# Optimization experiments

Hardware: AMD Instinct MI355X
Metric: run time of the kernel (lower is better)

Reference implementation:

```python
import jax, jax.numpy as jnp
import numpy as np

NA = 3          # anchors per head
NC = 3          # classes (labels < 3 are valid)
IGNORE_THRES = 0.5
OBJ_SCALE = 5.0
NOOBJ_SCALE = 0.5
GRIDS = [19, 38, 76]
SCALED_ANCHORS = [
    jnp.array([[116., 90.], [156., 198.], [373., 326.]], jnp.float32) / 32.0,  # large head
    jnp.array([[30., 61.], [62., 45.], [59., 119.]], jnp.float32) / 16.0,      # medium head
    jnp.array([[10., 13.], [16., 30.], [33., 23.]], jnp.float32) / 8.0,        # small head
]


def _safe_log(p):
    # torch BCELoss clamps log terms at -100
    return jnp.maximum(jnp.log(p), -100.0)


def _bce(p, t):
    return -(t * _safe_log(p) + (1.0 - t) * _safe_log(1.0 - p))


def _scale_loss(yolo_out, boxes, labels, anchors, G):
    B = yolo_out.shape[0]
    out = yolo_out.reshape(B, NA, G, G, -1)            # [B,3,G,G,8]
    aw = anchors[:, 0].reshape(1, NA, 1, 1)
    ah = anchors[:, 1].reshape(1, NA, 1, 1)
    # _change_bbox
    px = out[..., 0] - jnp.floor(out[..., 0])
    py = out[..., 1] - jnp.floor(out[..., 1])
    pw = jnp.log(out[..., 2] / aw + 1e-16)
    ph = jnp.log(out[..., 3] / ah + 1e-16)
    pconf = out[..., 4]
    pcls = out[..., 5:]                                 # [B,3,G,G,NC]
    # _yolo_targets (vectorized; boxes occupy distinct grid cells by construction)
    tb = boxes * G                                      # [B,nb,4]
    valid = labels < NC                                 # [B,nb]
    vf = valid.astype(out.dtype)
    gi = jnp.clip(tb[..., 0].astype(jnp.int32), 0, G - 1)
    gj = jnp.clip(tb[..., 1].astype(jnp.int32), 0, G - 1)
    bw, bh = tb[..., 2], tb[..., 3]                     # [B,nb]
    # anchor-wh IoU (same formula incl. 1e-16 placement as source)
    inter = jnp.minimum(anchors[:, 0], bw[..., None]) * jnp.minimum(anchors[:, 1], bh[..., None])
    union = anchors[:, 0] * anchors[:, 1] + 1e-16 + (bw * bh)[..., None] - inter
    iou = inter / union                                 # [B,nb,NA]
    best = jnp.argmax(iou, axis=-1)                     # [B,nb]
    bidx = jnp.arange(B)[:, None]                       # [B,1] -> broadcasts with [B,nb]
    obj = jnp.zeros((B, NA, G, G), out.dtype).at[bidx, best, gj, gi].max(vf)
    is_best = best[..., None] == jnp.arange(NA)         # [B,nb,NA]
    clear = valid[..., None] & ((iou > IGNORE_THRES) | is_best)
    keep = 1.0 - clear.astype(out.dtype)
    noobj = jnp.ones((B, NA, G, G), out.dtype).at[
        bidx[..., None], jnp.arange(NA), gj[..., None], gi[..., None]].min(keep)
    # tx/ty in the source are t_x - t_x.float() == 0, so targets stay zero
    twv = vf * jnp.log(bw / anchors[best, 0] + 1e-16)
    thv = vf * jnp.log(bh / anchors[best, 1] + 1e-16)
    tw = jnp.zeros((B, NA, G, G), out.dtype).at[bidx, best, gj, gi].set(twv)
    th = jnp.zeros((B, NA, G, G), out.dtype).at[bidx, best, gj, gi].set(thv)
    tcls = jnp.zeros((B, NA, G, G, NC), out.dtype).at[
        bidx, best, gj, gi, jnp.clip(labels, 0, NC - 1)].max(vf)
    tconf = obj
    # masked sum losses (reduction='sum' over masked elements)
    x_loss = jnp.sum(obj * px ** 2)
    y_loss = jnp.sum(obj * py ** 2)
    w_loss = jnp.sum(obj * (pw - tw) ** 2)
    h_loss = jnp.sum(obj * (ph - th) ** 2)
    conf_obj = jnp.sum(obj * _bce(pconf, tconf))
    conf_noobj = jnp.sum(noobj * _bce(pconf, tconf))
    cls_loss = jnp.sum(obj[..., None] * _bce(pcls, tcls))
    return (x_loss + y_loss + w_loss + h_loss
            + OBJ_SCALE * conf_obj + NOOBJ_SCALE * conf_noobj + cls_loss)


def reference(out_large, out_medium, out_small, boxes, labels):
    B = out_large.shape[0]
    loss = 0.0
    for out, anc, g in zip((out_large, out_medium, out_small), SCALED_ANCHORS, GRIDS):
        loss = loss + _scale_loss(out, boxes, labels, anc, g)
    return loss / B


def setup_inputs() -> dict:
    key = jax.random.key(0)
    ks = jax.random.split(key, 8)
    B, NB = 128, 12
    # predictions in (0.02, 0.98): valid BCE probs and positive w/h
    def u(k, shape):
        return 0.02 + 0.96 * jax.random.uniform(k, shape, jnp.float32)
    out_large = u(ks[0], (B, 3 * 19 * 19, 8))
    out_medium = u(ks[1], (B, 3 * 38 * 38, 8))
    out_small = u(ks[2], (B, 3 * 76 * 76, 8))
    # box centers: distinct grid columns per box at all grid sizes
    base_x = (jnp.arange(NB, dtype=jnp.float32) + 0.5) / NB
    xc = base_x[None, :] + jax.random.uniform(ks[3], (B, NB), jnp.float32, -0.004, 0.004)
    yc = jax.random.uniform(ks[4], (B, NB), jnp.float32, 0.1, 0.9)
    wh = jax.random.uniform(ks[5], (B, NB, 2), jnp.float32, 0.05, 0.4)
    boxes = jnp.concatenate([xc[..., None], yc[..., None], wh], axis=-1)
    labels = jax.random.randint(ks[6], (B, NB), 0, 5, jnp.int32)  # labels>=3 invalid
    return {"out_large": out_large, "out_medium": out_medium, "out_small": out_small,
            "boxes": boxes, "labels": labels}
```

## Files before the change

### kernel.cpp

```cpp
#include <hip/hip_runtime.h>

#define NA 3
#define NCLS 3
#define NB 12
#define BATCH 128
#define UNITS 1792

__device__ __constant__ float AWc[3][3] = {{3.625f, 4.875f, 11.65625f},
                                           {1.875f, 3.875f, 3.6875f},
                                           {1.25f,  2.0f,   4.125f}};
__device__ __constant__ float AHc[3][3] = {{2.8125f, 6.1875f, 10.1875f},
                                           {3.8125f, 2.8125f, 7.4375f},
                                           {1.625f,  3.75f,   2.875f}};

__device__ __forceinline__ float safelog(float x) {
    return fmaxf(__logf(x), -100.0f);
}


template <int G, int S>
__device__ __forceinline__ float cell_loss(int c, float4 q0, float4 q1,
                                           const int* rk, const float* sdat) {
    constexpr int GG = G * G;
    int a   = c / GG;
    int rem = c - a * GG;

    float keepv = 1.0f;
    int objn = -1;
#pragma unroll
    for (int n = 0; n < NB; n++) {
        int pk = rk[n];
        bool hit = ((pk & 0xFFFF) == rem);
        int fl = pk >> 16;
        if (hit && ((fl >> a) & 1)) keepv = 0.0f;
        if (hit && ((fl >> (4 + a)) & 1)) objn = n;
    }

    float conf = q1.x;
    float loss = -0.5f * keepv * safelog(1.0f - conf);

    if (objn >= 0) {
        int pk = rk[objn];
        int cls = (pk >> 24) & 3;
        float tw = sdat[objn], th = sdat[NB + objn];
        float aws = AWc[S][a], ahs = AHc[S][a];
        float px = q0.x - floorf(q0.x);
        float py = q0.y - floorf(q0.y);
        float pw = __logf(q0.z / aws + 1e-16f);
        float ph = __logf(q0.w / ahs + 1e-16f);
        float dw = pw - tw, dh = ph - th;
        loss += px * px + py * py + dw * dw + dh * dh;
        loss += -5.0f * safelog(conf);
        float c0 = q1.y, c1 = q1.z, c2 = q1.w;
        loss -= (cls == 0) ? safelog(c0) : safelog(1.0f - c0);
        loss -= (cls == 1) ? safelog(c1) : safelog(1.0f - c1);
        loss -= (cls == 2) ? safelog(c2) : safelog(1.0f - c2);
    }
    return loss;
}

template <int G, int S, int ITER>
__device__ __forceinline__ float scale_body(int b, int chunk,
        const float* __restrict__ outp,
        const float* __restrict__ boxes,
        const int* __restrict__ labels,
        int* skey, float* sdat)
{
    constexpr int GG = G * G;
    constexpr int CELLS = NA * GG;
    const int tid = threadIdx.x;

    if (tid < NB) {
        float4 bx = ((const float4*)boxes)[b * NB + tid];
        int lab = labels[b * NB + tid];
        bool valid = lab < NCLS;

        float bw = bx.z * (float)G, bh = bx.w * (float)G;
        int gi = min(max((int)(bx.x * (float)G), 0), G - 1);
        int gj = min(max((int)(bx.y * (float)G), 0), G - 1);

        float iou[3]; int best = 0; float bi = -1.0f;
#pragma unroll
        for (int a = 0; a < 3; a++) {
            float aw = AWc[S][a], ah = AHc[S][a];
            float inter = fminf(aw, bw) * fminf(ah, bh);
            float uni = aw * ah + 1e-16f + bw * bh - inter;
            iou[a] = inter / uni;
            if (iou[a] > bi) { bi = iou[a]; best = a; }
        }
        int flags = 0;
        if (valid) {
#pragma unroll
            for (int a = 0; a < 3; a++)
                if (iou[a] > 0.5f || a == best) flags |= (1 << a);
            flags |= (1 << (4 + best));
        }
        int cls = min(max(lab, 0), NCLS - 1);
        skey[tid] = (gj * G + gi) | (flags << 16) | (cls << 24);
        sdat[tid]      = valid ? __logf(bw / AWc[S][best] + 1e-16f) : 0.0f;
        sdat[NB + tid] = valid ? __logf(bh / AHc[S][best] + 1e-16f) : 0.0f;
    }
    __syncthreads();

    int rk[NB];
#pragma unroll
    for (int n = 0; n < NB; n++) rk[n] = __builtin_amdgcn_readfirstlane(skey[n]);

    const float* outb = outp + (size_t)b * CELLS * 8;
    float acc = 0.0f;
    const int base = chunk * (256 * ITER);

#pragma unroll
    for (int kb = 0; kb < ITER; kb += 4) {
        float4 Q0[4], Q1[4];
        int cs[4];
#pragma unroll
        for (int j = 0; j < 4; j++) {
            if (kb + j < ITER) {
                int c = base + (kb + j) * 256 + tid;
                cs[j] = c;
                int cc = (c < CELLS) ? c : (CELLS - 1);
                const float* cp = outb + (size_t)cc * 8;
                Q0[j] = *(const float4*)cp;
                Q1[j] = *(const float4*)(cp + 4);
            }
        }
#pragma unroll
        for (int j = 0; j < 4; j++) {
            if (kb + j < ITER) {
                float L = cell_loss<G, S>((cs[j] < CELLS) ? cs[j] : (CELLS - 1),
                                          Q0[j], Q1[j], rk, sdat);
                acc += (cs[j] < CELLS) ? L : 0.0f;
            }
        }
    }
    return acc;
}

__launch_bounds__(256)
__global__ void fused_loss(const float* __restrict__ oL,
                           const float* __restrict__ oM,
                           const float* __restrict__ oS,
                           const float* __restrict__ boxes,
                           const int* __restrict__ labels,
                           float* __restrict__ partials)
{
    __shared__ int skey[NB];
    __shared__ float sdat[2 * NB];
    __shared__ float red[256];

    const int u = blockIdx.x;
    const int tid = threadIdx.x;

    float acc;
    if (u < 128) {
        acc = scale_body<19, 0, 5>(u, 0, oL, boxes, labels, skey, sdat);
    } else if (u < 640) {
        int r = u - 128;
        acc = scale_body<38, 1, 5>(r >> 2, r & 3, oM, boxes, labels, skey, sdat);
    } else {
        int r = u - 640;
        acc = scale_body<76, 2, 8>(r / 9, r % 9, oS, boxes, labels, skey, sdat);
    }

    red[tid] = acc;
    __syncthreads();
#pragma unroll
    for (int s = 128; s > 0; s >>= 1) {
        if (tid < s) red[tid] += red[tid + s];
        __syncthreads();
    }
    if (tid == 0) partials[u] = red[0];
}

__global__ void final_reduce(const float* __restrict__ partials,
                             float* __restrict__ out) {
    __shared__ float red[256];
    const int tid = threadIdx.x;
    float acc = 0.0f;
#pragma unroll
    for (int i = 0; i < 7; i++) acc += partials[tid + i * 256];
    red[tid] = acc;
    __syncthreads();
#pragma unroll
    for (int s = 128; s > 0; s >>= 1) {
        if (tid < s) red[tid] += red[tid + s];
        __syncthreads();
    }
    if (tid == 0) out[0] = red[0] * (1.0f / (float)BATCH);
}

extern "C" void kernel_launch(void* const* d_in, const int* in_sizes, int n_in,
                              void* d_out, int out_size, void* d_ws, size_t ws_size,
                              hipStream_t stream) {
    const float* oL     = (const float*)d_in[0];
    const float* oM     = (const float*)d_in[1];
    const float* oS     = (const float*)d_in[2];
    const float* boxes  = (const float*)d_in[3];
    const int*   labels = (const int*)d_in[4];

    float* partials = (float*)d_ws;

    fused_loss<<<UNITS, 256, 0, stream>>>(oL, oM, oS, boxes, labels, partials);
    final_reduce<<<1, 256, 0, stream>>>(partials, (float*)d_out);
}
```

Measured before the change: 25.55 us.

## Split loss into dense no-object stream plus sparse per-box corrections

Measured after the change: 24.76 us. 3.1% less time.

```diff
diff --git a/kernel.cpp b/kernel.cpp
--- a/kernel.cpp
+++ b/kernel.cpp
@@ -4,7 +4,16 @@
 #define NCLS 3
 #define NB 12
 #define BATCH 128
-#define UNITS 1792
+
+#define NL_CELLS (128 * 1083)
+#define NM_CELLS (128 * 4332)
+#define NS_CELLS (128 * 17328)
+#define NTOT (NL_CELLS + NM_CELLS + NS_CELLS)
+
+#define CORR_BLOCKS 384
+#define STREAM_BLOCKS 1536
+#define UNITS (CORR_BLOCKS + STREAM_BLOCKS)
+#define STRIDE (STREAM_BLOCKS * 256)
 
 __device__ __constant__ float AWc[3][3] = {{3.625f, 4.875f, 11.65625f},
                                            {1.875f, 3.875f, 3.6875f},
@@ -17,124 +26,75 @@
     return fmaxf(__logf(x), -100.0f);
 }
 
+template <int G, int S>
+__device__ __forceinline__ float corr_body(int b, const float* __restrict__ outp,
+                                           const float* __restrict__ boxes,
+                                           const int* __restrict__ labels) {
+    constexpr int GG = G * G;
+    constexpr int CELLS = NA * GG;
+    const int l = threadIdx.x;
+    const int n = l / 3, a = l - n * 3;
+    const bool active = (l < 36);
+    const int nn = active ? n : 0;
 
-template <int G, int S>
-__device__ __forceinline__ float cell_loss(int c, float4 q0, float4 q1,
-                                           const int* rk, const float* sdat) {
-    constexpr int GG = G * G;
-    int a   = c / GG;
-    int rem = c - a * GG;
+    float4 bx = ((const float4*)boxes)[b * NB + nn];
+    int lab = labels[b * NB + nn];
+    bool valid = active && (lab < NCLS);
 
-    float keepv = 1.0f;
-    int objn = -1;
+    float bw = bx.z * (float)G, bh = bx.w * (float)G;
+    int gi = min(max((int)(bx.x * (float)G), 0), G - 1);
+    int gj = min(max((int)(bx.y * (float)G), 0), G - 1);
+
+    float iou[3]; int best = 0; float bi = -1.0f;
 #pragma unroll
-    for (int n = 0; n < NB; n++) {
-        int pk = rk[n];
-        bool hit = ((pk & 0xFFFF) == rem);
-        int fl = pk >> 16;
-        if (hit && ((fl >> a) & 1)) keepv = 0.0f;
-        if (hit && ((fl >> (4 + a)) & 1)) objn = n;
+    for (int aa = 0; aa < 3; aa++) {
+        float aw = AWc[S][aa], ah = AHc[S][aa];
+        float inter = fminf(aw, bw) * fminf(ah, bh);
+        float uni = aw * ah + 1e-16f + bw * bh - inter;
+        iou[aa] = inter / uni;
+        if (iou[aa] > bi) { bi = iou[aa]; best = aa; }
+    }
+    bool cleared = valid && (iou[a] > 0.5f || a == best);
+    bool isobj   = valid && (a == best);
+
+    unsigned key = (unsigned)(a * GG + gj * G + gi);
+    unsigned v = key | (cleared ? 0x100000u : 0u) | (isobj ? 0x200000u : 0u);
+
+    bool dupc = false, notwin = false;
+#pragma unroll
+    for (int j = 0; j < 36; j++) {
+        unsigned vj = (unsigned)__shfl((int)v, j);
+        bool same = ((vj ^ v) & 0xFFFFFu) == 0u;
+        dupc   = dupc   || (same && (vj & 0x100000u) && j < l);
+        notwin = notwin || (same && (vj & 0x200000u) && j > l);
     }
 
-    float conf = q1.x;
-    float loss = -0.5f * keepv * safelog(1.0f - conf);
+    float corr = 0.0f;
+    const float* cellp = outp + ((size_t)b * CELLS + key) * 8;
 
-    if (objn >= 0) {
-        int pk = rk[objn];
-        int cls = (pk >> 24) & 3;
-        float tw = sdat[objn], th = sdat[NB + objn];
-        float aws = AWc[S][a], ahs = AHc[S][a];
+    if (cleared && !dupc) {
+        float conf = cellp[4];
+        corr += 0.5f * safelog(1.0f - conf);
+    }
+    if (isobj && !notwin) {
+        float4 q0 = *(const float4*)cellp;
+        float4 q1 = *(const float4*)(cellp + 4);
+        float aw = AWc[S][a], ah = AHc[S][a];
+        float tw = __logf(bw / aw + 1e-16f);
+        float th = __logf(bh / ah + 1e-16f);
         float px = q0.x - floorf(q0.x);
         float py = q0.y - floorf(q0.y);
-        float pw = __logf(q0.z / aws + 1e-16f);
-        float ph = __logf(q0.w / ahs + 1e-16f);
+        float pw = __logf(q0.z / aw + 1e-16f);
+        float ph = __logf(q0.w / ah + 1e-16f);
         float dw = pw - tw, dh = ph - th;
-        loss += px * px + py * py + dw * dw + dh * dh;
-        loss += -5.0f * safelog(conf);
-        float c0 = q1.y, c1 = q1.z, c2 = q1.w;
-        loss -= (cls == 0) ? safelog(c0) : safelog(1.0f - c0);
-        loss -= (cls == 1) ? safelog(c1) : safelog(1.0f - c1);
-        loss -= (cls == 2) ? safelog(c2) : safelog(1.0f - c2);
+        float conf = q1.x;
+        corr += px * px + py * py + dw * dw + dh * dh;
+        corr -= 5.0f * safelog(conf);
+        corr -= (lab == 0) ? safelog(q1.y) : safelog(1.0f - q1.y);
+        corr -= (lab == 1) ? safelog(q1.z) : safelog(1.0f - q1.z);
+        corr -= (lab == 2) ? safelog(q1.w) : safelog(1.0f - q1.w);
     }
-    return loss;
-}
-
-template <int G, int S, int ITER>
-__device__ __forceinline__ float scale_body(int b, int chunk,
-        const float* __restrict__ outp,
-        const float* __restrict__ boxes,
-        const int* __restrict__ labels,
-        int* skey, float* sdat)
-{
-    constexpr int GG = G * G;
-    constexpr int CELLS = NA * GG;
-    const int tid = threadIdx.x;
-
-    if (tid < NB) {
-        float4 bx = ((const float4*)boxes)[b * NB + tid];
-        int lab = labels[b * NB + tid];
-        bool valid = lab < NCLS;
-
-        float bw = bx.z * (float)G, bh = bx.w * (float)G;
-        int gi = min(max((int)(bx.x * (float)G), 0), G - 1);
-        int gj = min(max((int)(bx.y * (float)G), 0), G - 1);
-
-        float iou[3]; int best = 0; float bi = -1.0f;
-#pragma unroll
-        for (int a = 0; a < 3; a++) {
-            float aw = AWc[S][a], ah = AHc[S][a];
-            float inter = fminf(aw, bw) * fminf(ah, bh);
-            float uni = aw * ah + 1e-16f + bw * bh - inter;
-            iou[a] = inter / uni;
-            if (iou[a] > bi) { bi = iou[a]; best = a; }
-        }
-        int flags = 0;
-        if (valid) {
-#pragma unroll
-            for (int a = 0; a < 3; a++)
-                if (iou[a] > 0.5f || a == best) flags |= (1 << a);
-            flags |= (1 << (4 + best));
-        }
-        int cls = min(max(lab, 0), NCLS - 1);
-        skey[tid] = (gj * G + gi) | (flags << 16) | (cls << 24);
-        sdat[tid]      = valid ? __logf(bw / AWc[S][best] + 1e-16f) : 0.0f;
-        sdat[NB + tid] = valid ? __logf(bh / AHc[S][best] + 1e-16f) : 0.0f;
-    }
-    __syncthreads();
-
-    int rk[NB];
-#pragma unroll
-    for (int n = 0; n < NB; n++) rk[n] = __builtin_amdgcn_readfirstlane(skey[n]);
-
-    const float* outb = outp + (size_t)b * CELLS * 8;
-    float acc = 0.0f;
-    const int base = chunk * (256 * ITER);
-
-#pragma unroll
-    for (int kb = 0; kb < ITER; kb += 4) {
-        float4 Q0[4], Q1[4];
-        int cs[4];
-#pragma unroll
-        for (int j = 0; j < 4; j++) {
-            if (kb + j < ITER) {
-                int c = base + (kb + j) * 256 + tid;
-                cs[j] = c;
-                int cc = (c < CELLS) ? c : (CELLS - 1);
-                const float* cp = outb + (size_t)cc * 8;
-                Q0[j] = *(const float4*)cp;
-                Q1[j] = *(const float4*)(cp + 4);
-            }
-        }
-#pragma unroll
-        for (int j = 0; j < 4; j++) {
-            if (kb + j < ITER) {
-                float L = cell_loss<G, S>((cs[j] < CELLS) ? cs[j] : (CELLS - 1),
-                                          Q0[j], Q1[j], rk, sdat);
-                acc += (cs[j] < CELLS) ? L : 0.0f;
-            }
-        }
-    }
-    return acc;
+    return corr;
 }
 
 __launch_bounds__(256)
@@ -145,22 +105,38 @@
                            const int* __restrict__ labels,
                            float* __restrict__ partials)
 {
-    __shared__ int skey[NB];
-    __shared__ float sdat[2 * NB];
     __shared__ float red[256];
-
     const int u = blockIdx.x;
     const int tid = threadIdx.x;
+    float acc = 0.0f;
 
-    float acc;
-    if (u < 128) {
-        acc = scale_body<19, 0, 5>(u, 0, oL, boxes, labels, skey, sdat);
-    } else if (u < 640) {
-        int r = u - 128;
-        acc = scale_body<38, 1, 5>(r >> 2, r & 3, oM, boxes, labels, skey, sdat);
+    if (u < CORR_BLOCKS) {
+        int s = u >> 7, b = u & 127;
+        if (tid < 64) {
+            if      (s == 0) acc = corr_body<19, 0>(b, oL, boxes, labels);
+            else if (s == 1) acc = corr_body<38, 1>(b, oM, boxes, labels);
+            else             acc = corr_body<76, 2>(b, oS, boxes, labels);
+        }
     } else {
-        int r = u - 640;
-        acc = scale_body<76, 2, 8>(r / 9, r % 9, oS, boxes, labels, skey, sdat);
+        const int g0 = (u - CORR_BLOCKS) * 256 + tid;
+        float cv[8];
+        int ids[8];
+#pragma unroll
+        for (int k = 0; k < 8; k++) {
+            int id = g0 + k * STRIDE;
+            ids[k] = id;
+            int idc = (id < NTOT) ? id : (NTOT - 1);
+            const float* p; int off;
+            if (idc < NL_CELLS)                { p = oL; off = idc; }
+            else if (idc < NL_CELLS + NM_CELLS){ p = oM; off = idc - NL_CELLS; }
+            else                               { p = oS; off = idc - NL_CELLS - NM_CELLS; }
+            cv[k] = p[(size_t)off * 8 + 4];
+        }
+#pragma unroll
+        for (int k = 0; k < 8; k++) {
+            float t = -0.5f * safelog(1.0f - cv[k]);
+            acc += (ids[k] < NTOT) ? t : 0.0f;
+        }
     }
 
     red[tid] = acc;
@@ -178,8 +154,7 @@
     __shared__ float red[256];
     const int tid = threadIdx.x;
     float acc = 0.0f;
-#pragma unroll
-    for (int i = 0; i < 7; i++) acc += partials[tid + i * 256];
+    for (int i = tid; i < UNITS; i += 256) acc += partials[i];
     red[tid] = acc;
     __syncthreads();
 #pragma unroll
```
